# Kernel tuning notes

Hardware: AMD Instinct MI355X
Metric: run time of the kernel (lower is better)

## Reference

```python
import jax, jax.numpy as jnp
import numpy as np

N, E, G, H, D = 50000, 800000, 64, 2, 128  # nodes, edges, graphs, heads, out_channels
NEG_SLOPE_ATT = 0.2   # GATv2 default negative_slope
NEG_SLOPE_OUT = 0.01  # torch.nn.LeakyReLU default
BN_EPS = 1e-5


def setup_inputs() -> dict:
    key = jax.random.key(0)
    ks = jax.random.split(key, 12)
    x = jax.random.normal(ks[0], (N, 1), jnp.float32)
    edge_index = jax.random.randint(ks[1], (2, E), 0, N, dtype=jnp.int64)
    edge_attr = jax.random.normal(ks[2], (E,), jnp.float32)
    batch = jnp.sort(jax.random.randint(ks[3], (N,), 0, G, dtype=jnp.int64))
    # GATv2Conv params: lin_l/lin_r: Linear(1, H*D) with bias; lin_edge: Linear(1, H*D) no bias
    Wl = jax.random.normal(ks[4], (1, H * D), jnp.float32) * 0.5
    bl = jax.random.normal(ks[5], (H * D,), jnp.float32) * 0.1
    Wr = jax.random.normal(ks[6], (1, H * D), jnp.float32) * 0.5
    br = jax.random.normal(ks[7], (H * D,), jnp.float32) * 0.1
    We = jax.random.normal(ks[8], (1, H * D), jnp.float32) * 0.5
    att = jax.random.normal(ks[9], (H, D), jnp.float32) * 0.5
    bias = jax.random.normal(ks[10], (D,), jnp.float32) * 0.1
    gamma = jnp.ones((D,), jnp.float32)
    beta = jnp.zeros((D,), jnp.float32)
    return {"x": x, "edge_index": edge_index, "edge_attr": edge_attr, "batch": batch,
            "Wl": Wl, "bl": bl, "Wr": Wr, "br": br, "We": We, "att": att,
            "bias": bias, "gamma": gamma, "beta": beta}


def reference(x, edge_index, edge_attr, batch, Wl, bl, Wr, br, We, att, bias, gamma, beta):
    n = x.shape[0]
    src, dst = edge_index[0], edge_index[1]  # message flows src -> dst
    # node transforms: [N, H, D]
    xl = (x @ Wl + bl).reshape(n, H, D)  # lin_l (source side, also the message value)
    xr = (x @ Wr + br).reshape(n, H, D)  # lin_r (destination side)
    # edge feature embedding: [E, H, D]
    ee = (edge_attr[:, None] @ We).reshape(-1, H, D)
    # GATv2 scoring: leaky_relu(x_j + x_i + e), then dot with attention vector
    m = jax.nn.leaky_relu(xl[src] + xr[dst] + ee, NEG_SLOPE_ATT)  # [E, H, D]
    alpha = jnp.einsum('ehd,hd->eh', m, att)  # [E, H]
    # scatter-softmax over incoming edges per destination node
    amax = jax.ops.segment_max(alpha, dst, num_segments=n)  # [N, H]
    ea = jnp.exp(alpha - amax[dst])
    denom = jax.ops.segment_sum(ea, dst, num_segments=n)
    alpha = ea / (denom[dst] + 1e-16)
    # weighted scatter-add aggregation of x_j
    out = jax.ops.segment_sum(xl[src] * alpha[..., None], dst, num_segments=n)  # [N, H, D]
    out = out.mean(axis=1) + bias  # concat=False -> head average, then conv bias
    # BatchNorm1d in training mode (biased variance over nodes)
    mean = out.mean(axis=0)
    var = ((out - mean) ** 2).mean(axis=0)
    out = (out - mean) * jax.lax.rsqrt(var + BN_EPS) * gamma + beta
    out = jax.nn.leaky_relu(out, NEG_SLOPE_OUT)
    # graph-level scatter_add pooling
    return jax.ops.segment_sum(out, batch, num_segments=G)  # [G, D]
```

## Files before the change

kernel.cpp:

```cpp
#include <hip/hip_runtime.h>
#include <math.h>

#define NN 50000
#define NE 800000
#define NG 64

#define WS_C     0
#define WS_ACC   16
#define WS_BNSUM (WS_ACC + 4*NN)
#define WS_BNSQ  (WS_BNSUM + 128)
#define WS_HEAD  (WS_BNSQ + 128)
#define WS_STAGE (WS_HEAD + NN)
#define WS_END   (WS_STAGE + 4*NE)
#define WS_NEED_BYTES ((size_t)WS_END * 4 + 256)

static_assert(((WS_STAGE * 4) % 16) == 0, "stage 16B alignment");
static_assert(NE % 4 == 0, "edge unroll");

extern "C" __global__ __launch_bounds__(256)
void k0_init(float* __restrict__ ws,
             const float* __restrict__ att, const float* __restrict__ Wl,
             const float* __restrict__ Wr, const float* __restrict__ We,
             const float* __restrict__ bl, const float* __restrict__ br,
             float* __restrict__ out)
{
  int tid = blockIdx.x * 256 + threadIdx.x;
  int nt = gridDim.x * 256;
  for (int i = tid; i < 4 * NN; i += nt) ws[WS_ACC + i] = 0.f;
  for (int i = tid; i < 256; i += nt) ws[WS_BNSUM + i] = 0.f;
  for (int i = tid; i < NG * 128; i += nt) out[i] = 0.f;
  unsigned* head = (unsigned*)(ws + WS_HEAD);
  for (int i = tid; i < NN; i += nt) head[i] = 0xFFFFFFFFu;
  if (blockIdx.x == 0) {
    __shared__ float red[4][256];
    int t = threadIdx.x;
    float a = att[t];
    red[0][t] = a * Wl[t];
    red[1][t] = a * Wr[t];
    red[2][t] = a * We[t];
    red[3][t] = a * (bl[t] + br[t]);
    __syncthreads();
    if (t < 8) {
      int k = t >> 1, h = t & 1;
      float s = 0.f;
      for (int d = 0; d < 128; ++d) s += red[k][h * 128 + d];
      ws[WS_C + h * 4 + k] = s;
    }
  }
}

#define STEP(wl_, wr_, we_, bb_, at_, xs_, xd_, ae_, acc_)                 \
  { float tt = fmaf(we_, ae_, bb_); tt = fmaf(wr_, xd_, tt);               \
    tt = fmaf(wl_, xs_, tt); acc_ = fmaf(fabsf(tt), at_, acc_); }

#define STEP4(c, q0, q1, q2, q3)                                           \
  STEP(wl.c, wr.c, we.c, bb.c, at.c, xs0, xd0, ae0, q0)                    \
  STEP(wl.c, wr.c, we.c, bb.c, at.c, xs1, xd1, ae1, q1)                    \
  STEP(wl.c, wr.c, we.c, bb.c, at.c, xs2, xd2, ae2, q2)                    \
  STEP(wl.c, wr.c, we.c, bb.c, at.c, xs3, xd3, ae3, q3)

#define SCORE_PREAMBLE                                                     \
  __shared__ __align__(16) float sWl[256], sWr[256], sWe[256], sB[256], sAt[256]; \
  { int t = threadIdx.x;                                                   \
    sWl[t] = Wl[t]; sWr[t] = Wr[t]; sWe[t] = We[t];                        \
    sB[t] = bl[t] + br[t]; sAt[t] = att[t]; }                              \
  __syncthreads();                                                         \
  int base = (blockIdx.x * 256 + threadIdx.x) * 4;                         \
  if (base >= NE) return;                                                  \
  int4 s4 = *(const int4*)&ei[base];                                       \
  int4 dd4 = *(const int4*)&ei[NE + base];                                 \
  float4 ae4 = *(const float4*)&eattr[base];                               \
  float xs0 = x[s4.x], xs1 = x[s4.y], xs2 = x[s4.z], xs3 = x[s4.w];        \
  float xd0 = x[dd4.x], xd1 = x[dd4.y], xd2 = x[dd4.z], xd3 = x[dd4.w];    \
  float ae0 = ae4.x, ae1 = ae4.y, ae2 = ae4.z, ae3 = ae4.w;                \
  float a00 = 0.f, a01 = 0.f, a02 = 0.f, a03 = 0.f;                        \
  float a10 = 0.f, a11 = 0.f, a12 = 0.f, a13 = 0.f;                        \
  _Pragma("unroll 2")                                                      \
  for (int j = 0; j < 128; j += 4) {                                       \
    float4 wl = *(const float4*)&sWl[j];                                   \
    float4 wr = *(const float4*)&sWr[j];                                   \
    float4 we = *(const float4*)&sWe[j];                                   \
    float4 bb = *(const float4*)&sB[j];                                    \
    float4 at = *(const float4*)&sAt[j];                                   \
    STEP4(x, a00, a01, a02, a03)                                           \
    STEP4(y, a00, a01, a02, a03)                                           \
    STEP4(z, a00, a01, a02, a03)                                           \
    STEP4(w, a00, a01, a02, a03)                                           \
  }                                                                        \
  _Pragma("unroll 2")                                                      \
  for (int j = 128; j < 256; j += 4) {                                     \
    float4 wl = *(const float4*)&sWl[j];                                   \
    float4 wr = *(const float4*)&sWr[j];                                   \
    float4 we = *(const float4*)&sWe[j];                                   \
    float4 bb = *(const float4*)&sB[j];                                    \
    float4 at = *(const float4*)&sAt[j];                                   \
    STEP4(x, a10, a11, a12, a13)                                           \
    STEP4(y, a10, a11, a12, a13)                                           \
    STEP4(z, a10, a11, a12, a13)                                           \
    STEP4(w, a10, a11, a12, a13)                                           \
  }                                                                        \
  float4 c0 = *(const float4*)&ws[WS_C];                                   \
  float4 c1 = *(const float4*)&ws[WS_C + 4];

#define SCORES(xs_, xd_, ae_, accA, accB, out0, out1)                      \
  { float lin0 = fmaf(c0.x, xs_, fmaf(c0.y, xd_, fmaf(c0.z, ae_, c0.w))); \
    out0 = fmaf(0.4f, accA, 0.6f * lin0);                                  \
    float lin1 = fmaf(c1.x, xs_, fmaf(c1.y, xd_, fmaf(c1.z, ae_, c1.w))); \
    out1 = fmaf(0.4f, accB, 0.6f * lin1); }

extern "C" __global__ __launch_bounds__(256)
void ke_edge(const int* __restrict__ ei, const float* __restrict__ x,
             const float* __restrict__ eattr,
             const float* __restrict__ Wl, const float* __restrict__ Wr,
             const float* __restrict__ We, const float* __restrict__ bl,
             const float* __restrict__ br, const float* __restrict__ att,
             float* __restrict__ ws)
{
  SCORE_PREAMBLE
  unsigned* head = (unsigned*)(ws + WS_HEAD);
  float4* stage = (float4*)(ws + WS_STAGE);
  float s0, s1;
#define EPI(xs_, xd_, ae_, accA, accB, dsti, eoff)                         \
  { SCORES(xs_, xd_, ae_, accA, accB, s0, s1)                              \
    float e0 = __expf(s0), e1 = __expf(s1);                                \
    unsigned prev = atomicExch(&head[dsti], (unsigned)(base + eoff));      \
    stage[base + eoff] = make_float4(e0, e1, xs_, __uint_as_float(prev)); }
  EPI(xs0, xd0, ae0, a00, a10, dd4.x, 0)
  EPI(xs1, xd1, ae1, a01, a11, dd4.y, 1)
  EPI(xs2, xd2, ae2, a02, a12, dd4.z, 2)
  EPI(xs3, xd3, ae3, a03, a13, dd4.w, 3)
#undef EPI
}

extern "C" __global__ __launch_bounds__(256)
void kf_gather(float* __restrict__ ws)
{
  int n = blockIdx.x * 256 + threadIdx.x;
  if (n >= NN) return;
  const unsigned* head = (const unsigned*)(ws + WS_HEAD);
  const float4* stage = (const float4*)(ws + WS_STAGE);
  unsigned p = head[n];
  float den0 = 0.f, den1 = 0.f, t10 = 0.f, t11 = 0.f;
  while (p != 0xFFFFFFFFu) {
    float4 q = stage[p];
    den0 += q.x; den1 += q.y;
    t10 = fmaf(q.x, q.z, t10);
    t11 = fmaf(q.y, q.z, t11);
    p = __float_as_uint(q.w);
  }
  *(float4*)&ws[WS_ACC + 4 * n] = make_float4(den0, den1, t10, t11);
}

extern "C" __global__ __launch_bounds__(256)
void k12f(const int* __restrict__ ei, const float* __restrict__ x,
          const float* __restrict__ eattr,
          const float* __restrict__ Wl, const float* __restrict__ Wr,
          const float* __restrict__ We, const float* __restrict__ bl,
          const float* __restrict__ br, const float* __restrict__ att,
          float* __restrict__ ws)
{
  SCORE_PREAMBLE
  float* acc = ws + WS_ACC;
  float s0, s1;
#define EPI2(xs_, xd_, ae_, accA, accB, dsti)                              \
  { SCORES(xs_, xd_, ae_, accA, accB, s0, s1)                              \
    float e0 = __expf(s0), e1 = __expf(s1);                                \
    float* a = &acc[4 * dsti];                                             \
    atomicAdd(a + 0, e0); atomicAdd(a + 1, e1);                            \
    atomicAdd(a + 2, e0 * xs_); atomicAdd(a + 3, e1 * xs_); }
  EPI2(xs0, xd0, ae0, a00, a10, dd4.x)
  EPI2(xs1, xd1, ae1, a01, a11, dd4.y)
  EPI2(xs2, xd2, ae2, a02, a12, dd4.z)
  EPI2(xs3, xd3, ae3, a03, a13, dd4.w)
#undef EPI2
}

__device__ __forceinline__ float node_out4(float4 a, float wl0, float wl1,
                                           float b0, float b1, float bs)
{
  float r0 = 1.f / (a.x + 1e-16f);
  float r1 = 1.f / (a.y + 1e-16f);
  return 0.5f * (fmaf(wl0, a.z * r0, b0 * (a.x * r0)) +
                 fmaf(wl1, a.w * r1, b1 * (a.y * r1))) + bs;
}

extern "C" __global__ __launch_bounds__(256)
void k3_stats(const float* __restrict__ Wl, const float* __restrict__ bl,
              const float* __restrict__ bias, float* __restrict__ ws)
{
  int d = threadIdx.x & 127;
  int row = threadIdx.x >> 7;
  float wl0 = Wl[d], wl1 = Wl[128 + d];
  float b0 = bl[d], b1 = bl[128 + d];
  float bs = bias[d];
  float sum = 0.f, sq = 0.f;
  for (int n = blockIdx.x * 2 + row; n < NN; n += gridDim.x * 2) {
    float4 a = *(const float4*)&ws[WS_ACC + 4 * n];
    float o = node_out4(a, wl0, wl1, b0, b1, bs);
    sum += o;
    sq = fmaf(o, o, sq);
  }
  __shared__ float l1[256], l2[256];
  l1[threadIdx.x] = sum; l2[threadIdx.x] = sq;
  __syncthreads();
  if (row == 0) {
    atomicAdd(&ws[WS_BNSUM + d], l1[d] + l1[128 + d]);
    atomicAdd(&ws[WS_BNSQ + d], l2[d] + l2[128 + d]);
  }
}

extern "C" __global__ __launch_bounds__(256)
void k4_pool(const int* __restrict__ batch,
             const float* __restrict__ Wl, const float* __restrict__ bl,
             const float* __restrict__ bias, const float* __restrict__ gamma,
             const float* __restrict__ beta,
             float* __restrict__ ws, float* __restrict__ out)
{
  const int CHUNK = (NN + (int)gridDim.x - 1) / (int)gridDim.x;
  int n0 = blockIdx.x * CHUNK;
  if (n0 >= NN) return;
  int n1 = n0 + CHUNK; if (n1 > NN) n1 = NN;
  int d = threadIdx.x & 127;
  int row = threadIdx.x >> 7;
  const float invN = 1.f / (float)NN;
  float mean = ws[WS_BNSUM + d] * invN;
  float var = fmaf(ws[WS_BNSQ + d], invN, -mean * mean);
  float scale = gamma[d] * rsqrtf(var + 1e-5f);
  float shift = fmaf(-mean, scale, beta[d]);
  float wl0 = Wl[d], wl1 = Wl[128 + d];
  float b0 = bl[d], b1 = bl[128 + d];
  float bs = bias[d];
  __shared__ float pool[4][128];
  for (int i = threadIdx.x; i < 512; i += 256) ((float*)pool)[i] = 0.f;
  __syncthreads();
  int g0 = batch[n0];
  for (int n = n0 + row; n < n1; n += 2) {
    float4 a = *(const float4*)&ws[WS_ACC + 4 * n];
    float o = node_out4(a, wl0, wl1, b0, b1, bs);
    float v = fmaf(o, scale, shift);
    v = v > 0.f ? v : 0.01f * v;
    int g = batch[n];
    int slot = g - g0;
    if (slot < 4) atomicAdd(&pool[slot][d], v);
    else atomicAdd(&out[g * 128 + d], v);
  }
  __syncthreads();
  for (int i = threadIdx.x; i < 512; i += 256) {
    int slot = i >> 7, dd = i & 127;
    int g = g0 + slot;
    float v = pool[slot][dd];
    if (g < NG && v != 0.f) atomicAdd(&out[g * 128 + dd], v);
  }
}

extern "C" void kernel_launch(void* const* d_in, const int* in_sizes, int n_in,
                              void* d_out, int out_size, void* d_ws, size_t ws_size,
                              hipStream_t stream) {
  const float* x     = (const float*)d_in[0];
  const int*   ei    = (const int*)d_in[1];
  const float* eattr = (const float*)d_in[2];
  const int*   batch = (const int*)d_in[3];
  const float* Wl    = (const float*)d_in[4];
  const float* bl    = (const float*)d_in[5];
  const float* Wr    = (const float*)d_in[6];
  const float* br    = (const float*)d_in[7];
  const float* We    = (const float*)d_in[8];
  const float* att   = (const float*)d_in[9];
  const float* bias  = (const float*)d_in[10];
  const float* gam   = (const float*)d_in[11];
  const float* bet   = (const float*)d_in[12];
  float* ws  = (float*)d_ws;
  float* out = (float*)d_out;

  const bool dense = (ws_size >= WS_NEED_BYTES);
  const int EB = (NE / 4 + 255) / 256;

  hipLaunchKernelGGL(k0_init, dim3(128), dim3(256), 0, stream,
                     ws, att, Wl, Wr, We, bl, br, out);
  if (dense) {
    hipLaunchKernelGGL(ke_edge, dim3(EB), dim3(256), 0, stream,
                       ei, x, eattr, Wl, Wr, We, bl, br, att, ws);
    hipLaunchKernelGGL(kf_gather, dim3((NN + 255) / 256), dim3(256), 0, stream, ws);
  } else {
    hipLaunchKernelGGL(k12f, dim3(EB), dim3(256), 0, stream,
                       ei, x, eattr, Wl, Wr, We, bl, br, att, ws);
  }
  hipLaunchKernelGGL(k3_stats, dim3(256), dim3(256), 0, stream,
                     Wl, bl, bias, ws);
  hipLaunchKernelGGL(k4_pool, dim3(256), dim3(256), 0, stream,
                     batch, Wl, bl, bias, gam, bet, ws, out);
}
```

Baseline: 229.0 us.

## Split per-node linked lists into four interleaved chains for parallel gather

Each destination node now keeps four list heads, one per edge lane, so the gather kernel walks four independent chains at once. This shortens the dependent pointer-chasing latency per node. The next-pointers move to a separate array, the atomic exchanges are issued before the score loops so their latency overlaps the compute, and e*xs is precomputed into the stage payload. In exchange the head array and workspace grow, and the gather loop gains extra branches.

New measurement: 229.5 us. No clear change (+0.2%).

```diff
diff --git a/kernel.cpp b/kernel.cpp
--- a/kernel.cpp
+++ b/kernel.cpp
@@ -10,9 +10,12 @@
 #define WS_BNSUM (WS_ACC + 4*NN)
 #define WS_BNSQ  (WS_BNSUM + 128)
 #define WS_HEAD  (WS_BNSQ + 128)
-#define WS_STAGE (WS_HEAD + NN)
+#define WS_PREV  (WS_HEAD + 4*NN)
+#define WS_STAGE (WS_PREV + NE)
 #define WS_END   (WS_STAGE + 4*NE)
 #define WS_NEED_BYTES ((size_t)WS_END * 4 + 256)
+
+#define LEND 0xFFFFFFFFu
 
 static_assert(((WS_STAGE * 4) % 16) == 0, "stage 16B alignment");
 static_assert(NE % 4 == 0, "edge unroll");
@@ -22,15 +25,18 @@
              const float* __restrict__ att, const float* __restrict__ Wl,
              const float* __restrict__ Wr, const float* __restrict__ We,
              const float* __restrict__ bl, const float* __restrict__ br,
-             float* __restrict__ out)
+             float* __restrict__ out, int dense)
 {
   int tid = blockIdx.x * 256 + threadIdx.x;
   int nt = gridDim.x * 256;
-  for (int i = tid; i < 4 * NN; i += nt) ws[WS_ACC + i] = 0.f;
+  if (dense) {
+    unsigned* head = (unsigned*)(ws + WS_HEAD);
+    for (int i = tid; i < 4 * NN; i += nt) head[i] = LEND;
+  } else {
+    for (int i = tid; i < 4 * NN; i += nt) ws[WS_ACC + i] = 0.f;
+  }
   for (int i = tid; i < 256; i += nt) ws[WS_BNSUM + i] = 0.f;
   for (int i = tid; i < NG * 128; i += nt) out[i] = 0.f;
-  unsigned* head = (unsigned*)(ws + WS_HEAD);
-  for (int i = tid; i < NN; i += nt) head[i] = 0xFFFFFFFFu;
   if (blockIdx.x == 0) {
     __shared__ float red[4][256];
     int t = threadIdx.x;
@@ -59,20 +65,15 @@
   STEP(wl.c, wr.c, we.c, bb.c, at.c, xs2, xd2, ae2, q2)                    \
   STEP(wl.c, wr.c, we.c, bb.c, at.c, xs3, xd3, ae3, q3)
 
-#define SCORE_PREAMBLE                                                     \
-  __shared__ __align__(16) float sWl[256], sWr[256], sWe[256], sB[256], sAt[256]; \
-  { int t = threadIdx.x;                                                   \
-    sWl[t] = Wl[t]; sWr[t] = Wr[t]; sWe[t] = We[t];                        \
-    sB[t] = bl[t] + br[t]; sAt[t] = att[t]; }                              \
-  __syncthreads();                                                         \
-  int base = (blockIdx.x * 256 + threadIdx.x) * 4;                         \
-  if (base >= NE) return;                                                  \
+#define SCORE_CORE                                                         \
   int4 s4 = *(const int4*)&ei[base];                                       \
   int4 dd4 = *(const int4*)&ei[NE + base];                                 \
   float4 ae4 = *(const float4*)&eattr[base];                               \
   float xs0 = x[s4.x], xs1 = x[s4.y], xs2 = x[s4.z], xs3 = x[s4.w];        \
   float xd0 = x[dd4.x], xd1 = x[dd4.y], xd2 = x[dd4.z], xd3 = x[dd4.w];    \
-  float ae0 = ae4.x, ae1 = ae4.y, ae2 = ae4.z, ae3 = ae4.w;                \
+  float ae0 = ae4.x, ae1 = ae4.y, ae2 = ae4.z, ae3 = ae4.w;
+
+#define SCORE_LOOPS                                                        \
   float a00 = 0.f, a01 = 0.f, a02 = 0.f, a03 = 0.f;                        \
   float a10 = 0.f, a11 = 0.f, a12 = 0.f, a13 = 0.f;                        \
   _Pragma("unroll 2")                                                      \
@@ -102,6 +103,13 @@
   float4 c0 = *(const float4*)&ws[WS_C];                                   \
   float4 c1 = *(const float4*)&ws[WS_C + 4];
 
+#define SMEM_WEIGHTS                                                       \
+  __shared__ __align__(16) float sWl[256], sWr[256], sWe[256], sB[256], sAt[256]; \
+  { int t = threadIdx.x;                                                   \
+    sWl[t] = Wl[t]; sWr[t] = Wr[t]; sWe[t] = We[t];                        \
+    sB[t] = bl[t] + br[t]; sAt[t] = att[t]; }                              \
+  __syncthreads();
+
 #define SCORES(xs_, xd_, ae_, accA, accB, out0, out1)                      \
   { float lin0 = fmaf(c0.x, xs_, fmaf(c0.y, xd_, fmaf(c0.z, ae_, c0.w))); \
     out0 = fmaf(0.4f, accA, 0.6f * lin0);                                  \
@@ -116,20 +124,34 @@
              const float* __restrict__ br, const float* __restrict__ att,
              float* __restrict__ ws)
 {
-  SCORE_PREAMBLE
+  SMEM_WEIGHTS
+  int base = (blockIdx.x * 256 + threadIdx.x) * 4;
+  if (base >= NE) return;
+  SCORE_CORE
   unsigned* head = (unsigned*)(ws + WS_HEAD);
+  unsigned pv0 = atomicExch(&head[4 * dd4.x + 0], (unsigned)(base + 0));
+  unsigned pv1 = atomicExch(&head[4 * dd4.y + 1], (unsigned)(base + 1));
+  unsigned pv2 = atomicExch(&head[4 * dd4.z + 2], (unsigned)(base + 2));
+  unsigned pv3 = atomicExch(&head[4 * dd4.w + 3], (unsigned)(base + 3));
+  SCORE_LOOPS
   float4* stage = (float4*)(ws + WS_STAGE);
+  unsigned* prev = (unsigned*)(ws + WS_PREV);
   float s0, s1;
-#define EPI(xs_, xd_, ae_, accA, accB, dsti, eoff)                         \
+  float4 pay0, pay1, pay2, pay3;
+#define PAY(xs_, xd_, ae_, accA, accB, pp)                                 \
   { SCORES(xs_, xd_, ae_, accA, accB, s0, s1)                              \
     float e0 = __expf(s0), e1 = __expf(s1);                                \
-    unsigned prev = atomicExch(&head[dsti], (unsigned)(base + eoff));      \
-    stage[base + eoff] = make_float4(e0, e1, xs_, __uint_as_float(prev)); }
-  EPI(xs0, xd0, ae0, a00, a10, dd4.x, 0)
-  EPI(xs1, xd1, ae1, a01, a11, dd4.y, 1)
-  EPI(xs2, xd2, ae2, a02, a12, dd4.z, 2)
-  EPI(xs3, xd3, ae3, a03, a13, dd4.w, 3)
-#undef EPI
+    pp = make_float4(e0, e1, e0 * xs_, e1 * xs_); }
+  PAY(xs0, xd0, ae0, a00, a10, pay0)
+  PAY(xs1, xd1, ae1, a01, a11, pay1)
+  PAY(xs2, xd2, ae2, a02, a12, pay2)
+  PAY(xs3, xd3, ae3, a03, a13, pay3)
+#undef PAY
+  stage[base + 0] = pay0;
+  stage[base + 1] = pay1;
+  stage[base + 2] = pay2;
+  stage[base + 3] = pay3;
+  *(uint4*)&prev[base] = make_uint4(pv0, pv1, pv2, pv3);
 }
 
 extern "C" __global__ __launch_bounds__(256)
@@ -138,17 +160,28 @@
   int n = blockIdx.x * 256 + threadIdx.x;
   if (n >= NN) return;
   const unsigned* head = (const unsigned*)(ws + WS_HEAD);
+  const unsigned* prev = (const unsigned*)(ws + WS_PREV);
   const float4* stage = (const float4*)(ws + WS_STAGE);
-  unsigned p = head[n];
-  float den0 = 0.f, den1 = 0.f, t10 = 0.f, t11 = 0.f;
-  while (p != 0xFFFFFFFFu) {
-    float4 q = stage[p];
-    den0 += q.x; den1 += q.y;
-    t10 = fmaf(q.x, q.z, t10);
-    t11 = fmaf(q.y, q.z, t11);
-    p = __float_as_uint(q.w);
-  }
-  *(float4*)&ws[WS_ACC + 4 * n] = make_float4(den0, den1, t10, t11);
+  uint4 p = *(const uint4*)&head[4 * n];
+  float4 A0 = make_float4(0.f, 0.f, 0.f, 0.f);
+  float4 A1 = A0, A2 = A0, A3 = A0;
+  while ((p.x & p.y & p.z & p.w) != LEND) {
+#define HOP(pc, Ac)                                                        \
+    if (pc != LEND) {                                                      \
+      float4 q = stage[pc];                                                \
+      unsigned np = prev[pc];                                              \
+      Ac.x += q.x; Ac.y += q.y; Ac.z += q.z; Ac.w += q.w;                  \
+      pc = np;                                                             \
+    }
+    HOP(p.x, A0) HOP(p.y, A1) HOP(p.z, A2) HOP(p.w, A3)
+#undef HOP
+  }
+  float4 r;
+  r.x = (A0.x + A1.x) + (A2.x + A3.x);
+  r.y = (A0.y + A1.y) + (A2.y + A3.y);
+  r.z = (A0.z + A1.z) + (A2.z + A3.z);
+  r.w = (A0.w + A1.w) + (A2.w + A3.w);
+  *(float4*)&ws[WS_ACC + 4 * n] = r;
 }
 
 extern "C" __global__ __launch_bounds__(256)
@@ -159,7 +192,11 @@
           const float* __restrict__ br, const float* __restrict__ att,
           float* __restrict__ ws)
 {
-  SCORE_PREAMBLE
+  SMEM_WEIGHTS
+  int base = (blockIdx.x * 256 + threadIdx.x) * 4;
+  if (base >= NE) return;
+  SCORE_CORE
+  SCORE_LOOPS
   float* acc = ws + WS_ACC;
   float s0, s1;
 #define EPI2(xs_, xd_, ae_, accA, accB, dsti)                              \
@@ -276,7 +313,7 @@
   const int EB = (NE / 4 + 255) / 256;
 
   hipLaunchKernelGGL(k0_init, dim3(128), dim3(256), 0, stream,
-                     ws, att, Wl, Wr, We, bl, br, out);
+                     ws, att, Wl, Wr, We, bl, br, out, dense ? 1 : 0);
   if (dense) {
     hipLaunchKernelGGL(ke_edge, dim3(EB), dim3(256), 0, stream,
                        ei, x, eattr, Wl, Wr, We, bl, br, att, ws);
```
